# Kernel optimization log

Hardware: AMD Instinct MI355X
Metric: run time of the kernel (lower is better)

The kernel has to match this reference:

```python
import jax, jax.numpy as jnp
import numpy as np

D_MODEL = 1024
N_HEADS = 16
D_HEAD = D_MODEL // N_HEADS


def setup_inputs() -> dict:
    key = jax.random.key(0)
    k_x, k_w1, k_b1, k_w2, k_b2 = jax.random.split(key, 5)
    B, T = 4, 2048
    s1 = 1.0 / np.sqrt(D_MODEL)
    return {
        "x": jax.random.normal(k_x, (B, T, D_MODEL), dtype=jnp.float32),
        # torch nn.Linear: weight [out,in], y = x @ W.T + b
        "qkv_w": jax.random.uniform(k_w1, (3 * D_MODEL, D_MODEL), minval=-s1, maxval=s1, dtype=jnp.float32),
        "qkv_b": jax.random.uniform(k_b1, (3 * D_MODEL,), minval=-s1, maxval=s1, dtype=jnp.float32),
        "out_w": jax.random.uniform(k_w2, (D_MODEL, D_MODEL), minval=-s1, maxval=s1, dtype=jnp.float32),
        "out_b": jax.random.uniform(k_b2, (D_MODEL,), minval=-s1, maxval=s1, dtype=jnp.float32),
    }


def reference(x, qkv_w, qkv_b, out_w, out_b):
    B, T, C = x.shape
    qkv = x @ qkv_w.T + qkv_b                      # [B,T,3C]
    qkv = qkv.reshape(B, T, 3, N_HEADS, D_HEAD)
    qkv = jnp.transpose(qkv, (2, 0, 3, 1, 4))      # [3,B,H,T,Dh]
    q, k, v = qkv[0], qkv[1], qkv[2]
    scale = 1.0 / np.sqrt(D_HEAD).astype(np.float32)
    attn = jnp.einsum("bhqd,bhkd->bhqk", q, k) * scale
    causal = jnp.tril(jnp.ones((T, T), dtype=bool))
    attn = jnp.where(causal[None, None], attn, -jnp.inf)
    attn_weights = jax.nn.softmax(attn, axis=-1)   # [B,H,T,T]
    out = jnp.einsum("bhqk,bhkd->bhqd", attn_weights, v)
    out = jnp.transpose(out, (0, 2, 1, 3)).reshape(B, T, C)
    out = out @ out_w.T + out_b
    return out, attn_weights
```

## Files before the change

### kernel.cpp

```cpp
#include <hip/hip_runtime.h>

typedef __bf16 bf16x8 __attribute__((ext_vector_type(8)));
typedef float f32x4 __attribute__((ext_vector_type(4)));
typedef int i32x4 __attribute__((ext_vector_type(4)));

#define DEV __device__ __forceinline__
#define AS1 __attribute__((address_space(1)))
#define AS3 __attribute__((address_space(3)))

DEV unsigned short f2bf(float f) {
  union { float f; unsigned u; } x; x.f = f;
  unsigned r = x.u + 0x7fffu + ((x.u >> 16) & 1u);
  return (unsigned short)(r >> 16);
}

DEV unsigned pkbf(float a, float b) {
  unsigned r;
  asm("v_cvt_pk_bf16_f32 %0, %1, %2" : "=v"(r) : "v"(a), "v"(b));
  return r;
}

DEV f32x4 mfma16(bf16x8 a, bf16x8 b, f32x4 c) {
  return __builtin_amdgcn_mfma_f32_16x16x32_bf16(a, b, c, 0, 0, 0);
}

#if __has_builtin(__builtin_amdgcn_exp2f)
DEV float xexp2(float x) { return __builtin_amdgcn_exp2f(x); }
#else
DEV float xexp2(float x) { return __expf(x * 0.6931471805599453f); }
#endif

DEV void gload16(const void* g, void* lds) {
  __builtin_amdgcn_global_load_lds((const AS1 void*)g, (AS3 void*)lds, 16, 0, 0);
}

__global__ void f2b_kernel(const float* __restrict__ src, unsigned short* __restrict__ dst, int n) {
  int i = (blockIdx.x * blockDim.x + threadIdx.x) * 4;
  int stride = gridDim.x * blockDim.x * 4;
  for (; i < n; i += stride) {
    float4 v = *reinterpret_cast<const float4*>(src + i);
    ushort4 o;
    o.x = f2bf(v.x); o.y = f2bf(v.y); o.z = f2bf(v.z); o.w = f2bf(v.w);
    *reinterpret_cast<ushort4*>(dst + i) = o;
  }
}

template <int EPI>
__global__ __launch_bounds__(256, 2)
void gemm_bt(const unsigned short* __restrict__ A, const unsigned short* __restrict__ B,
             const float* __restrict__ bias, void* __restrict__ outv,
             int M, int N, int K) {
  __shared__ __align__(16) unsigned short As[128 * 64];
  __shared__ __align__(16) unsigned short Bs[128 * 64];
  const int tid = threadIdx.x;
  const int l = tid & 63, w = tid >> 6;
  const int wr = w >> 1, wc = w & 1;
  const int tm = blockIdx.x * 128, tn = blockIdx.y * 128;
  const int lr = l >> 3, lc = (l & 7) * 8;

  f32x4 acc[4][4] = {};

  for (int kt = 0; kt < K; kt += 64) {
#pragma unroll
    for (int i = 0; i < 4; ++i) {
      int c = i * 4 + w;
      gload16(A + (size_t)(tm + c * 8 + lr) * K + kt + lc, (char*)As + c * 1024);
    }
#pragma unroll
    for (int i = 0; i < 4; ++i) {
      int c = i * 4 + w;
      gload16(B + (size_t)(tn + c * 8 + lr) * K + kt + lc, (char*)Bs + c * 1024);
    }
    __syncthreads();
#pragma unroll
    for (int ks = 0; ks < 2; ++ks) {
      int ko = ks * 32 + (l >> 4) * 8;
      bf16x8 af[4], bfr[4];
#pragma unroll
      for (int i = 0; i < 4; ++i) {
        af[i]  = *reinterpret_cast<const bf16x8*>(As + (wr * 64 + i * 16 + (l & 15)) * 64 + ko);
        bfr[i] = *reinterpret_cast<const bf16x8*>(Bs + (wc * 64 + i * 16 + (l & 15)) * 64 + ko);
      }
#pragma unroll
      for (int mi = 0; mi < 4; ++mi)
#pragma unroll
        for (int ni = 0; ni < 4; ++ni)
          acc[mi][ni] = mfma16(af[mi], bfr[ni], acc[mi][ni]);
    }
    __syncthreads();
  }

#pragma unroll
  for (int ni = 0; ni < 4; ++ni) {
    int n = tn + wc * 64 + ni * 16 + (l & 15);
    float bv = bias[n];
    if (EPI == 0) {
      float* out = (float*)outv;
#pragma unroll
      for (int mi = 0; mi < 4; ++mi)
#pragma unroll
        for (int r = 0; r < 4; ++r) {
          int m = tm + wr * 64 + mi * 16 + (l >> 4) * 4 + r;
          out[(size_t)m * N + n] = acc[mi][ni][r] + bv;
        }
    } else {
      unsigned short* out = (unsigned short*)outv;
      int s = n >> 10, rem = n & 1023, h = rem >> 6, d = rem & 63;
      if (s == 2) {
#pragma unroll
        for (int mi = 0; mi < 4; ++mi) {
          int m = tm + wr * 64 + mi * 16 + (l >> 4) * 4;
          int bb = m >> 11, t = m & 2047;
          ushort4 pv;
          pv.x = f2bf(acc[mi][ni][0] + bv);
          pv.y = f2bf(acc[mi][ni][1] + bv);
          pv.z = f2bf(acc[mi][ni][2] + bv);
          pv.w = f2bf(acc[mi][ni][3] + bv);
          size_t off = ((size_t)(128 + bb * 16 + h)) * 131072 + (size_t)d * 2048 + t;
          *reinterpret_cast<ushort4*>(out + off) = pv;
        }
      } else {
        const float sc = (s == 0) ? 0.1803368801f : 1.0f;
#pragma unroll
        for (int mi = 0; mi < 4; ++mi)
#pragma unroll
          for (int r = 0; r < 4; ++r) {
            int m = tm + wr * 64 + mi * 16 + (l >> 4) * 4 + r;
            int bb = m >> 11, t = m & 2047;
            size_t off = ((((size_t)s * 4 + bb) * 16 + h) * 2048 + t) * 64 + d;
            out[off] = f2bf((acc[mi][ni][r] + bv) * sc);
          }
      }
    }
  }
}

__global__ __launch_bounds__(256, 3)
void attn_kernel(const unsigned short* __restrict__ qkv, float* __restrict__ attnW,
                 unsigned short* __restrict__ Ob) {
  __shared__ __align__(16) char smem[49152];

  const int tid = threadIdx.x, l = tid & 63, w = tid >> 6;
  const int li = l & 15, g = l >> 4;
  const int dd = blockIdx.x;
  const int bh = (dd & 7) + ((dd >> 3) & 7) * 8;
  const int qt = 15 - (dd >> 6);
  const int b = bh >> 4, hh = bh & 15;
  const size_t plane = (size_t)2048 * 64;
  const unsigned short* Qg  = qkv + (size_t)bh * plane;
  const unsigned short* Kg  = qkv + ((size_t)64 + bh) * plane;
  const unsigned short* VTg = qkv + ((size_t)128 + bh) * plane;
  const int q0 = qt * 128;
  const int nkt = 2 * qt + 2;

  bf16x8 bq[2][2];
#pragma unroll
  for (int qB = 0; qB < 2; ++qB)
#pragma unroll
    for (int ks = 0; ks < 2; ++ks) {
      int cc = ks * 4 + g;
      bq[qB][ks] = *reinterpret_cast<const bf16x8*>(
          Qg + (size_t)(q0 + w * 32 + qB * 16 + li) * 64 + cc * 8);
    }

  auto stageK = [&](int kt, char* base) {
#pragma unroll
    for (int it = 0; it < 2; ++it) {
      int c = it * 4 + w;
      int X = c * 1024 + l * 16;
      int row = X >> 7, sl = (X >> 4) & 7;
      gload16(Kg + (size_t)(kt * 64 + row) * 64 + ((sl ^ (row & 7)) * 8), base + c * 1024);
    }
  };
  auto stageVT = [&](int kt, char* base) {
#pragma unroll
    for (int it = 0; it < 2; ++it) {
      int c = it * 4 + w;
      int X = c * 1024 + l * 16;
      int row = X >> 7, sl = (X >> 4) & 7;
      gload16(VTg + (size_t)row * 2048 + kt * 64 + ((sl ^ (row & 7)) * 8), base + c * 1024);
    }
  };

  auto computeS = [&](const char* base, f32x4 s[4][2]) {
    const unsigned short* Kp = (const unsigned short*)base;
#pragma unroll
    for (int ks = 0; ks < 2; ++ks) {
      bf16x8 ak[4];
      int cc = ks * 4 + g;
#pragma unroll
      for (int kA = 0; kA < 4; ++kA) {
        int kr = kA * 16 + li;
        ak[kA] = *reinterpret_cast<const bf16x8*>(Kp + kr * 64 + ((cc ^ (kr & 7)) * 8));
      }
#pragma unroll
      for (int kA = 0; kA < 4; ++kA)
#pragma unroll
        for (int qB = 0; qB < 2; ++qB)
          s[kA][qB] = mfma16(ak[kA], bq[qB][ks], s[kA][qB]);
    }
  };

  float lsum[2] = {0.f, 0.f};
  {
    int i0 = 0, i1 = 1, i2 = 2;
    stageK(0, smem);
    stageK(1, smem + 8192);
    asm volatile("s_waitcnt vmcnt(2)" ::: "memory");
    asm volatile("s_barrier" ::: "memory");
    for (int kt = 0; kt < nkt; ++kt) {
      const bool pf = (kt + 2 < nkt);
      if (pf) stageK(kt + 2, smem + i2 * 8192);
      f32x4 s[4][2] = {};
      computeS(smem + i0 * 8192, s);
      const bool dg = (kt >= 2 * qt);
#pragma unroll
      for (int qB = 0; qB < 2; ++qB) {
        int qg = q0 + w * 32 + qB * 16 + li;
        float a = 0.f;
#pragma unroll
        for (int kA = 0; kA < 4; ++kA)
#pragma unroll
          for (int r = 0; r < 4; ++r) {
            float e = xexp2(s[kA][qB][r]);
            if (dg) { int k = kt * 64 + kA * 16 + g * 4 + r; e = (k <= qg) ? e : 0.f; }
            a += e;
          }
        lsum[qB] += a;
      }
      if (pf) asm volatile("s_waitcnt vmcnt(2)" ::: "memory");
      else    asm volatile("s_waitcnt vmcnt(0)" ::: "memory");
      asm volatile("s_barrier" ::: "memory");
      int t = i0; i0 = i1; i1 = i2; i2 = t;
    }
  }

  float linv[2];
#pragma unroll
  for (int qB = 0; qB < 2; ++qB) {
    float v = lsum[qB];
    v += __shfl_xor(v, 16, 64);
    v += __shfl_xor(v, 32, 64);
    linv[qB] = 1.0f / v;
  }

  __syncthreads();
  char* KsB  = smem;
  char* VsB  = smem + 16384;
  unsigned short* PsW = (unsigned short*)(smem + 32768 + w * 4096);

  stageK(0, KsB);
  stageVT(0, VsB);
  asm volatile("" ::: "memory");
  asm volatile("s_waitcnt vmcnt(0)" ::: "memory");
  asm volatile("s_barrier" ::: "memory");

  f32x4 o[2][4] = {};
  int cb = 0;

  for (int kt = 0; kt < nkt; ++kt) {
    const int nb = cb ^ 1;
    if (kt + 1 < nkt) { stageK(kt + 1, KsB + nb * 8192); stageVT(kt + 1, VsB + nb * 8192); }
    asm volatile("" ::: "memory");

    f32x4 s[4][2] = {};
    computeS(KsB + cb * 8192, s);

    const bool dg = (kt >= 2 * qt);
#pragma unroll
    for (int kA = 0; kA < 4; ++kA)
#pragma unroll
      for (int qB = 0; qB < 2; ++qB) {
        int qg = q0 + w * 32 + qB * 16 + li;
        f32x4 e;
#pragma unroll
        for (int r = 0; r < 4; ++r) {
          float v = xexp2(s[kA][qB][r]) * linv[qB];
          if (dg) { int k = kt * 64 + kA * 16 + g * 4 + r; v = (k <= qg) ? v : 0.f; }
          e[r] = v;
        }
        __builtin_nontemporal_store(e, reinterpret_cast<f32x4*>(
            attnW + ((size_t)bh * 2048 + qg) * 2048 + kt * 64 + kA * 16 + g * 4));
        uint2 pk;
        pk.x = pkbf(e[0], e[1]);
        pk.y = pkbf(e[2], e[3]);
        int qr = qB * 16 + li;
        *reinterpret_cast<uint2*>((char*)PsW + qr * 128 + ((kA * 32 + g * 8) ^ ((qr & 7) << 4))) = pk;
      }

    __builtin_amdgcn_wave_barrier();

    const unsigned short* Vp = (const unsigned short*)(VsB + cb * 8192);
#pragma unroll
    for (int ks = 0; ks < 2; ++ks) {
      int cc = ks * 4 + g;
      bf16x8 av[4], bp[2];
#pragma unroll
      for (int df = 0; df < 4; ++df) {
        int dr = df * 16 + li;
        av[df] = *reinterpret_cast<const bf16x8*>(Vp + dr * 64 + ((cc ^ (dr & 7)) * 8));
      }
#pragma unroll
      for (int qB = 0; qB < 2; ++qB) {
        int qr = qB * 16 + li;
        bp[qB] = *reinterpret_cast<const bf16x8*>((const char*)PsW + qr * 128 + ((ks * 64 + g * 16) ^ ((qr & 7) << 4)));
      }
#pragma unroll
      for (int qB = 0; qB < 2; ++qB)
#pragma unroll
        for (int df = 0; df < 4; ++df)
          o[qB][df] = mfma16(av[df], bp[qB], o[qB][df]);
    }

    asm volatile("s_waitcnt vmcnt(8)" ::: "memory");
    asm volatile("s_barrier" ::: "memory");
    cb = nb;
  }

#pragma unroll
  for (int qB = 0; qB < 2; ++qB) {
    int qg = q0 + w * 32 + qB * 16 + li;
#pragma unroll
    for (int df = 0; df < 4; ++df) {
      ushort4 ov;
      ov.x = f2bf(o[qB][df][0]);
      ov.y = f2bf(o[qB][df][1]);
      ov.z = f2bf(o[qB][df][2]);
      ov.w = f2bf(o[qB][df][3]);
      *reinterpret_cast<ushort4*>(Ob + ((size_t)b * 2048 + qg) * 1024 + hh * 64 + df * 16 + g * 4) = ov;
    }
  }

  {
    int col0 = 128 * (qt + 1);
    int nch = (2048 - col0) >> 2;
    f32x4 z = {0.f, 0.f, 0.f, 0.f};
    for (int row = 0; row < 128; ++row) {
      size_t base = ((size_t)bh * 2048 + (q0 + row)) * 2048 + col0;
      for (int c = tid; c < nch; c += 256)
        __builtin_nontemporal_store(z, reinterpret_cast<f32x4*>(attnW + base + (size_t)c * 4));
    }
  }
}

extern "C" void kernel_launch(void* const* d_in, const int* in_sizes, int n_in,
                              void* d_out, int out_size, void* d_ws, size_t ws_size,
                              hipStream_t stream) {
  const float* x  = (const float*)d_in[0];
  const float* w1 = (const float*)d_in[1];
  const float* b1 = (const float*)d_in[2];
  const float* w2 = (const float*)d_in[3];
  const float* b2 = (const float*)d_in[4];
  float* out = (float*)d_out;
  float* attnW = out + (size_t)8192 * 1024;

  unsigned short* xb   = (unsigned short*)d_ws;
  unsigned short* w1b  = xb + (size_t)8192 * 1024;
  unsigned short* w2b  = w1b + (size_t)3072 * 1024;
  unsigned short* qkvb = w2b + (size_t)1024 * 1024;
  unsigned short* ob   = qkvb + (size_t)3 * 8192 * 1024;

  f2b_kernel<<<1024, 256, 0, stream>>>(x, xb, 8192 * 1024);
  f2b_kernel<<<512, 256, 0, stream>>>(w1, w1b, 3072 * 1024);
  f2b_kernel<<<256, 256, 0, stream>>>(w2, w2b, 1024 * 1024);

  gemm_bt<1><<<dim3(64, 24), 256, 0, stream>>>(xb, w1b, b1, qkvb, 8192, 3072, 1024);

  attn_kernel<<<1024, 256, 0, stream>>>(qkvb, attnW, ob);

  gemm_bt<0><<<dim3(64, 8), 256, 0, stream>>>(ob, w2b, b2, out, 8192, 1024, 1024);
}
```

Before: 459.5 us.

## Use 128-row double-buffered K tiles in softmax-sum pass; raise GEMM occupancy hint

The first attention pass, which computes the row sums of exp, now stages 128-row K tiles with double buffering instead of 64-row tiles in a triple-buffered ring. This halves the number of barrier and waitcnt rounds per query tile. The GEMM kernel's launch bounds go from 2 to 3 blocks per CU, which pushes the compiler to use fewer registers. Costs: each in-flight prefetch is larger, the causal mask now covers the whole last 128-wide tile, and the GEMM may spill registers.

```diff
diff --git a/kernel.cpp b/kernel.cpp
--- a/kernel.cpp
+++ b/kernel.cpp
@@ -46,7 +46,7 @@
 }
 
 template <int EPI>
-__global__ __launch_bounds__(256, 2)
+__global__ __launch_bounds__(256, 3)
 void gemm_bt(const unsigned short* __restrict__ A, const unsigned short* __restrict__ B,
              const float* __restrict__ bias, void* __restrict__ outv,
              int M, int N, int K) {
@@ -163,22 +163,31 @@
           Qg + (size_t)(q0 + w * 32 + qB * 16 + li) * 64 + cc * 8);
     }
 
-  auto stageK = [&](int kt, char* base) {
+  auto stageK = [&](int kt64, char* base) {
 #pragma unroll
     for (int it = 0; it < 2; ++it) {
       int c = it * 4 + w;
       int X = c * 1024 + l * 16;
       int row = X >> 7, sl = (X >> 4) & 7;
-      gload16(Kg + (size_t)(kt * 64 + row) * 64 + ((sl ^ (row & 7)) * 8), base + c * 1024);
+      gload16(Kg + (size_t)(kt64 * 64 + row) * 64 + ((sl ^ (row & 7)) * 8), base + c * 1024);
     }
   };
-  auto stageVT = [&](int kt, char* base) {
+  auto stageK128 = [&](int kt128, char* base) {
+#pragma unroll
+    for (int it = 0; it < 4; ++it) {
+      int c = it * 4 + w;
+      int X = c * 1024 + l * 16;
+      int row = X >> 7, sl = (X >> 4) & 7;
+      gload16(Kg + (size_t)(kt128 * 128 + row) * 64 + ((sl ^ (row & 7)) * 8), base + c * 1024);
+    }
+  };
+  auto stageVT = [&](int kt64, char* base) {
 #pragma unroll
     for (int it = 0; it < 2; ++it) {
       int c = it * 4 + w;
       int X = c * 1024 + l * 16;
       int row = X >> 7, sl = (X >> 4) & 7;
-      gload16(VTg + (size_t)row * 2048 + kt * 64 + ((sl ^ (row & 7)) * 8), base + c * 1024);
+      gload16(VTg + (size_t)row * 2048 + kt64 * 64 + ((sl ^ (row & 7)) * 8), base + c * 1024);
     }
   };
 
@@ -203,35 +212,37 @@
 
   float lsum[2] = {0.f, 0.f};
   {
-    int i0 = 0, i1 = 1, i2 = 2;
-    stageK(0, smem);
-    stageK(1, smem + 8192);
-    asm volatile("s_waitcnt vmcnt(2)" ::: "memory");
+    const int nkt1 = qt + 1;
+    stageK128(0, smem);
+    asm volatile("s_waitcnt vmcnt(0)" ::: "memory");
     asm volatile("s_barrier" ::: "memory");
-    for (int kt = 0; kt < nkt; ++kt) {
-      const bool pf = (kt + 2 < nkt);
-      if (pf) stageK(kt + 2, smem + i2 * 8192);
-      f32x4 s[4][2] = {};
-      computeS(smem + i0 * 8192, s);
-      const bool dg = (kt >= 2 * qt);
-#pragma unroll
-      for (int qB = 0; qB < 2; ++qB) {
-        int qg = q0 + w * 32 + qB * 16 + li;
-        float a = 0.f;
-#pragma unroll
-        for (int kA = 0; kA < 4; ++kA)
-#pragma unroll
-          for (int r = 0; r < 4; ++r) {
-            float e = xexp2(s[kA][qB][r]);
-            if (dg) { int k = kt * 64 + kA * 16 + g * 4 + r; e = (k <= qg) ? e : 0.f; }
-            a += e;
-          }
-        lsum[qB] += a;
-      }
-      if (pf) asm volatile("s_waitcnt vmcnt(2)" ::: "memory");
-      else    asm volatile("s_waitcnt vmcnt(0)" ::: "memory");
+    int cb1 = 0;
+    for (int kt = 0; kt < nkt1; ++kt) {
+      const int nb1 = cb1 ^ 1;
+      if (kt + 1 < nkt1) stageK128(kt + 1, smem + nb1 * 16384);
+      const bool dg = (kt == qt);
+#pragma unroll
+      for (int half = 0; half < 2; ++half) {
+        f32x4 s[4][2] = {};
+        computeS(smem + cb1 * 16384 + half * 8192, s);
+#pragma unroll
+        for (int qB = 0; qB < 2; ++qB) {
+          int qg = q0 + w * 32 + qB * 16 + li;
+          float a = 0.f;
+#pragma unroll
+          for (int kA = 0; kA < 4; ++kA)
+#pragma unroll
+            for (int r = 0; r < 4; ++r) {
+              float e = xexp2(s[kA][qB][r]);
+              if (dg) { int k = kt * 128 + half * 64 + kA * 16 + g * 4 + r; e = (k <= qg) ? e : 0.f; }
+              a += e;
+            }
+          lsum[qB] += a;
+        }
+      }
+      asm volatile("s_waitcnt vmcnt(0)" ::: "memory");
       asm volatile("s_barrier" ::: "memory");
-      int t = i0; i0 = i1; i1 = i2; i2 = t;
+      cb1 = nb1;
     }
   }
 
@@ -245,8 +256,8 @@
   }
 
   __syncthreads();
-  char* KsB  = smem;
-  char* VsB  = smem + 16384;
+  char* KsB = smem;
+  char* VsB = smem + 16384;
   unsigned short* PsW = (unsigned short*)(smem + 32768 + w * 4096);
 
   stageK(0, KsB);
```

Result: no change. 454.5 us (-1.1%).
